# Kernel optimization log

Measured on AMD Instinct MI355X. Metric: run time of the kernel, lower is better.

The kernel has to match this reference:

```python
import jax, jax.numpy as jnp
import numpy as np

C = 512        # concept_num
D = 256        # input_dim / embedding_dim
H = 512        # msg_hidden_dim
M = 256        # msg_output_dim
OH = 512       # hidden_dim
T = 2          # edge_type_num
E = C * (C - 1)  # fully-connected graph without self-loops = 261632


def _glorot(key, shape, fan_in):
    return jax.random.normal(key, shape, jnp.float32) / np.sqrt(fan_in).astype(np.float32)


def setup_inputs() -> dict:
    key = jax.random.key(0)
    ks = jax.random.split(key, 12)
    inputs = jax.random.normal(ks[0], (C, D), jnp.float32)
    rel_type = jax.random.uniform(ks[1], (E, T), jnp.float32)
    send_idx = jax.random.randint(ks[2], (E,), 0, C, jnp.int32)
    rec_idx = jax.random.randint(ks[3], (E,), 0, C, jnp.int32)
    # per-edge-type message MLP params, stacked over type dim
    W1 = _glorot(ks[4], (T, 2 * D, H), 2 * D)
    b1 = jnp.zeros((T, H), jnp.float32)
    W2 = _glorot(ks[5], (T, H, M), H)
    b2 = jnp.zeros((T, M), jnp.float32)
    # output MLP params
    Wo1 = _glorot(ks[6], (M, OH), M)
    bo1 = jnp.zeros((OH,), jnp.float32)
    Wo2 = _glorot(ks[7], (OH, OH), OH)
    bo2 = jnp.zeros((OH,), jnp.float32)
    Wo3 = _glorot(ks[8], (OH, D), OH)
    bo3 = jnp.zeros((D,), jnp.float32)
    return {"inputs": inputs, "rel_type": rel_type, "W1": W1, "b1": b1,
            "W2": W2, "b2": b2, "Wo1": Wo1, "bo1": bo1, "Wo2": Wo2,
            "bo2": bo2, "Wo3": Wo3, "bo3": bo3,
            "send_idx": send_idx, "rec_idx": rec_idx}


def reference(inputs, rel_type, W1, b1, W2, b2, Wo1, bo1, Wo2, bo2, Wo3, bo3,
              send_idx, rec_idx):
    # node2edge: one-hot sparse matmul == index gather
    senders = jnp.take(inputs, send_idx, axis=0)      # [E, D]
    receivers = jnp.take(inputs, rec_idx, axis=0)     # [E, D]
    pre_msg = jnp.concatenate([senders, receivers], axis=-1)  # [E, 2D]
    # per-edge-type MLPs, weighted-summed by rel_type (dropout=0 / eval mode)
    all_msgs = jnp.zeros((pre_msg.shape[0], M), jnp.float32)
    for i in range(T):
        msg = jax.nn.relu(pre_msg @ W1[i] + b1[i])    # [E, H]
        msg = jax.nn.relu(msg @ W2[i] + b2[i])        # [E, M]
        all_msgs = all_msgs + msg * rel_type[:, i:i + 1]
    # edge2node: transposed one-hot sparse matmul == scatter-add over receivers
    agg_msgs = jax.ops.segment_sum(all_msgs, rec_idx, num_segments=inputs.shape[0])  # [C, M]
    pred = jax.nn.relu(agg_msgs @ Wo1 + bo1)
    pred = jax.nn.relu(pred @ Wo2 + bo2)
    return pred @ Wo3 + bo3                           # [C, D]
```

## Files before the change

kernel.cpp:

```cpp
#include <hip/hip_runtime.h>

#define C_N   512
#define E_N   261632
#define CAP   768

typedef _Float16 f16;
typedef _Float16 f16x8_t __attribute__((ext_vector_type(8)));
typedef float    f32x16_t __attribute__((ext_vector_type(16)));

__global__ __launch_bounds__(256) void k_prep_all(
    const float* __restrict__ inputs, const float* __restrict__ W1,
    const float* __restrict__ b1, const float* __restrict__ W2,
    const float* __restrict__ Wo1, const float* __restrict__ Wo2, const float* __restrict__ Wo3,
    f16* __restrict__ SA, f16* __restrict__ RB, f16* __restrict__ W2p,
    f16* __restrict__ Wo1p, f16* __restrict__ Wo2p, f16* __restrict__ Wo3p,
    int* __restrict__ cnt, float* __restrict__ agg)
{
  __shared__ f16 wt[2][256][18];
  int bid = blockIdx.x;
  int tid = threadIdx.x;
  if (bid < 64) {
    int lane = tid & 63, w = tid >> 6;
    int hlf = lane >> 5, l31 = lane & 31;
    int br = bid & 7, bc = (bid >> 3) & 1, mi = bid >> 4;
    int t = mi >> 1, half = mi & 1;
    const float* Wsrc = W1 + (size_t)t * 512 * 512 + (size_t)half * 256 * 512;

    f32x16_t acc[2][2];
    #pragma unroll
    for (int rt = 0; rt < 2; rt++)
      #pragma unroll
      for (int ctl = 0; ctl < 2; ctl++)
        #pragma unroll
        for (int r = 0; r < 16; r++) acc[rt][ctl][r] = 0.f;

    #pragma unroll
    for (int i = 0; i < 4; i++) {
      int idx = tid + i * 256;
      int k = idx >> 6, n4 = idx & 63;
      float4 v = *(const float4*)&Wsrc[(size_t)k * 512 + bc * 256 + n4 * 4];
      wt[0][n4 * 4 + 0][k] = (f16)v.x;
      wt[0][n4 * 4 + 1][k] = (f16)v.y;
      wt[0][n4 * 4 + 2][k] = (f16)v.z;
      wt[0][n4 * 4 + 3][k] = (f16)v.w;
    }

    for (int kc = 0; kc < 16; kc++) {
      __syncthreads();
      if (kc + 1 < 16) {
        int b = (kc + 1) & 1;
        #pragma unroll
        for (int i = 0; i < 4; i++) {
          int idx = tid + i * 256;
          int k = idx >> 6, n4 = idx & 63;
          float4 v = *(const float4*)&Wsrc[(size_t)((kc + 1) * 16 + k) * 512 + bc * 256 + n4 * 4];
          wt[b][n4 * 4 + 0][k] = (f16)v.x;
          wt[b][n4 * 4 + 1][k] = (f16)v.y;
          wt[b][n4 * 4 + 2][k] = (f16)v.z;
          wt[b][n4 * 4 + 3][k] = (f16)v.w;
        }
      }
      f16x8_t af[2];
      #pragma unroll
      for (int rt = 0; rt < 2; rt++) {
        const float4* p = (const float4*)&inputs[(size_t)(br * 64 + rt * 32 + l31) * 256 + kc * 16 + hlf * 8];
        float4 u0 = p[0], u1 = p[1];
        af[rt] = (f16x8_t){(f16)u0.x, (f16)u0.y, (f16)u0.z, (f16)u0.w,
                           (f16)u1.x, (f16)u1.y, (f16)u1.z, (f16)u1.w};
      }
      int b = kc & 1;
      #pragma unroll
      for (int ctl = 0; ctl < 2; ctl++) {
        int n = (2 * w + ctl) * 32 + l31;
        f16x8_t bfr = *(const f16x8_t*)&wt[b][n][hlf * 8];
        #pragma unroll
        for (int rt = 0; rt < 2; rt++)
          acc[rt][ctl] = __builtin_amdgcn_mfma_f32_32x32x16_f16(af[rt], bfr, acc[rt][ctl], 0, 0, 0);
      }
    }
    f16* dst = (half == 0) ? SA : RB;
    #pragma unroll
    for (int ctl = 0; ctl < 2; ctl++) {
      int col = bc * 256 + (2 * w + ctl) * 32 + l31;
      float bias = (half == 1) ? b1[t * 512 + col] : 0.f;
      #pragma unroll
      for (int rt = 0; rt < 2; rt++)
        #pragma unroll
        for (int r = 0; r < 16; r++) {
          int row = br * 64 + rt * 32 + (r & 3) + 8 * (r >> 2) + 4 * hlf;
          dst[((size_t)(t * 512 + row)) * 512 + col] = (f16)(acc[rt][ctl][r] + bias);
        }
    }
  } else if (bid < 192) {
    int gid  = (bid - 64) * 256 + tid;
    int lane = gid & 63;
    int ct   = (gid >> 6) & 7;
    int kc   = (gid >> 9) & 31;
    int t    = gid >> 14;
    int n    = ct * 32 + (lane & 31);
    int k0   = kc * 16 + (lane >> 5) * 8;
    const float* src = W2 + (size_t)t * 512 * 256;
    f16x8_t v;
    #pragma unroll
    for (int j = 0; j < 8; j++) v[j] = (f16)src[(size_t)(k0 + j) * 256 + n];
    *(f16x8_t*)(W2p + (size_t)gid * 8) = v;
  } else if (bid < 256) {
    int gid  = (bid - 192) * 256 + tid;
    int lane = gid & 63;
    int ct   = (gid >> 6) & 15;
    int kc   = gid >> 10;
    int n    = ct * 32 + (lane & 31);
    int k0   = kc * 16 + (lane >> 5) * 8;
    f16x8_t v;
    #pragma unroll
    for (int j = 0; j < 8; j++) v[j] = (f16)Wo1[(size_t)(k0 + j) * 512 + n];
    *(f16x8_t*)(Wo1p + (size_t)gid * 8) = v;
  } else if (bid < 384) {
    int gid  = (bid - 256) * 256 + tid;
    int lane = gid & 63;
    int ct   = (gid >> 6) & 15;
    int kc   = gid >> 10;
    int n    = ct * 32 + (lane & 31);
    int k0   = kc * 16 + (lane >> 5) * 8;
    f16x8_t v;
    #pragma unroll
    for (int j = 0; j < 8; j++) v[j] = (f16)Wo2[(size_t)(k0 + j) * 512 + n];
    *(f16x8_t*)(Wo2p + (size_t)gid * 8) = v;
  } else if (bid < 448) {
    int gid  = (bid - 384) * 256 + tid;
    int lane = gid & 63;
    int ct   = (gid >> 6) & 7;
    int kc   = gid >> 9;
    int n    = ct * 32 + (lane & 31);
    int k0   = kc * 16 + (lane >> 5) * 8;
    f16x8_t v;
    #pragma unroll
    for (int j = 0; j < 8; j++) v[j] = (f16)Wo3[(size_t)(k0 + j) * 256 + n];
    *(f16x8_t*)(Wo3p + (size_t)gid * 8) = v;
  } else if (bid == 448) {
    for (int i = tid; i < 512 * 16; i += 256) cnt[i] = 0;
  } else {
    float4* a4 = (float4*)agg;
    for (int i = tid; i < 512 * 64; i += 256) a4[i] = make_float4(0.f, 0.f, 0.f, 0.f);
  }
}

__global__ __launch_bounds__(512) void k_scatter_d(const int* __restrict__ rec,
    const int* __restrict__ send, const float* __restrict__ rel,
    int* __restrict__ cnt, uint2* __restrict__ smeta)
{
  __shared__ int lh[512];
  __shared__ int lb[512];
  int b = blockIdx.x;
  int e0 = b * (E_N / 128);
  lh[threadIdx.x] = 0;
  __syncthreads();
  for (int i = threadIdx.x; i < E_N / 128; i += 512)
    atomicAdd(&lh[rec[e0 + i]], 1);
  __syncthreads();
  {
    int c = lh[threadIdx.x];
    lb[threadIdx.x] = c ? atomicAdd(&cnt[threadIdx.x * 16], c) : 0;
    lh[threadIdx.x] = 0;
  }
  __syncthreads();
  for (int i = threadIdx.x; i < E_N / 128; i += 512) {
    int e = e0 + i;
    int r = rec[e];
    int p = r * CAP + lb[r] + atomicAdd(&lh[r], 1);
    f16 r0 = (f16)rel[2 * (size_t)e];
    f16 r1 = (f16)rel[2 * (size_t)e + 1];
    unsigned pk = ((unsigned)__builtin_bit_cast(unsigned short, r1) << 16)
                |  (unsigned)__builtin_bit_cast(unsigned short, r0);
    smeta[p] = make_uint2((unsigned)send[e], pk);
  }
}

#define H1S2 264

__global__ __launch_bounds__(512, 4) void k_edges(
    const f16* __restrict__ SA, const f16* __restrict__ RB,
    const f16* __restrict__ W2p, const float* __restrict__ b2,
    const uint2* __restrict__ smeta, const int* __restrict__ cnt,
    float* __restrict__ agg)
{
  __shared__ f16   h1[128 * H1S2];
  __shared__ f16   rbs[2][512];
  __shared__ float b2s[2][256];
  __shared__ float aggL[256];
  __shared__ float relv[128][2];
  __shared__ int   sends[128];

  int c   = blockIdx.x;
  int ti  = blockIdx.y;
  int n_c = cnt[c * 16];
  if (ti * 128 >= n_c) return;

  int tid  = threadIdx.x;
  int lane = tid & 63;
  int w    = tid >> 6;
  int hlf  = lane >> 5;
  int l31  = lane & 31;
  int q5   = tid & 31;
  int rb0  = tid >> 5;

  if (tid < 128) {
    int t = tid >> 6, qq = tid & 63;
    *(f16x8_t*)&rbs[t][qq * 8] = *(const f16x8_t*)&RB[((size_t)(t * 512 + c)) * 512 + qq * 8];
  }
  if (tid < 256) aggL[tid] = 0.0f;
  { int t = (tid >> 8) & 1, col = tid & 255; b2s[t][col] = b2[t * 256 + col]; }

  int s0 = c * CAP + ti * 128;
  int nv = n_c - ti * 128; if (nv > 128) nv = 128;

  if (tid < 128) {
    if (tid < nv) {
      uint2 m = smeta[s0 + tid];
      sends[tid] = (int)m.x;
      relv[tid][0] = (float)__builtin_bit_cast(f16, (unsigned short)(m.y & 0xffffu));
      relv[tid][1] = (float)__builtin_bit_cast(f16, (unsigned short)(m.y >> 16));
    } else {
      sends[tid] = 0; relv[tid][0] = 0.f; relv[tid][1] = 0.f;
    }
  }
  __syncthreads();

  f16x8_t g[8];
  const f16x8_t* SAc = (const f16x8_t*)SA;
  const f16x8_t* Bp  = (const f16x8_t*)W2p;
  f32x16_t acc[4];

  #pragma unroll
  for (int j = 0; j < 8; j++)
    g[j] = SAc[(size_t)sends[rb0 + 16 * j] * 64 + q5];

  for (int ph = 0; ph < 4; ph++) {
    int t  = ph >> 1;
    int kh = ph & 1;

    {
      f16x8_t rbq = *(const f16x8_t*)&rbs[t][(kh * 32 + q5) * 8];
      #pragma unroll
      for (int j = 0; j < 8; j++) {
        int row = rb0 + 16 * j;
        f16x8_t hv;
        #pragma unroll
        for (int e = 0; e < 8; e++) {
          f16 v = (f16)(g[j][e] + rbq[e]);
          hv[e] = (v > (f16)0.0f) ? v : (f16)0.0f;
        }
        *(f16x8_t*)&h1[row * H1S2 + q5 * 8] = hv;
      }
    }
    __syncthreads();

    if (kh == 0) {
      #pragma unroll
      for (int rt = 0; rt < 4; rt++)
        #pragma unroll
        for (int r = 0; r < 16; r++) acc[rt][r] = 0.f;
    }

    f16x8_t bb[2];
    bb[0] = Bp[(size_t)(((t * 32 + kh * 16 + 0) * 8 + w) * 64 + lane)];
    bb[1] = Bp[(size_t)(((t * 32 + kh * 16 + 1) * 8 + w) * 64 + lane)];

    if (ph < 3) {
      int tn  = (ph + 1) >> 1;
      int khn = (ph + 1) & 1;
      #pragma unroll
      for (int j = 0; j < 8; j++)
        g[j] = SAc[(size_t)(tn * 512 + sends[rb0 + 16 * j]) * 64 + khn * 32 + q5];
    }

    for (int kc = 0; kc < 16; kc++) {
      int pb = kc & 1;
      #pragma unroll
      for (int rt = 0; rt < 4; rt++) {
        f16x8_t af = *(const f16x8_t*)&h1[(rt * 32 + l31) * H1S2 + kc * 16 + hlf * 8];
        acc[rt] = __builtin_amdgcn_mfma_f32_32x32x16_f16(af, bb[pb], acc[rt], 0, 0, 0);
      }
      if (kc + 2 < 16)
        bb[pb] = Bp[(size_t)(((t * 32 + kh * 16 + kc + 2) * 8 + w) * 64 + lane)];
    }

    if (kh == 1) {
      int col = w * 32 + l31;
      float b2c = b2s[t][col];
      float csum = 0.0f;
      #pragma unroll
      for (int rt = 0; rt < 4; rt++)
        #pragma unroll
        for (int r = 0; r < 16; r++) {
          int row = rt * 32 + (r & 3) + 8 * (r >> 2) + 4 * hlf;
          float v = fmaxf(acc[rt][r] + b2c, 0.0f);
          csum += v * relv[row][t];
        }
      csum += __shfl_xor(csum, 32, 64);
      if (hlf == 0) aggL[col] += csum;
    }
    __syncthreads();
  }

  if (tid < 256) atomicAdd(&agg[(size_t)c * 256 + tid], aggL[tid]);
}

#define HOS 520

__global__ __launch_bounds__(512, 1) void k_omlp(const float* __restrict__ agg,
    const f16* __restrict__ Wo1p, const float* __restrict__ bo1,
    const f16* __restrict__ Wo2p, const float* __restrict__ bo2,
    const f16* __restrict__ Wo3p, const float* __restrict__ bo3,
    float* __restrict__ out)
{
  __shared__ f16 hL1[32 * HOS];
  __shared__ f16 hL2[32 * HOS];
  int tid = threadIdx.x, lane = tid & 63, w = tid >> 6;
  int hlf = lane >> 5, l31 = lane & 31;
  int br = blockIdx.x;

  {
    f32x16_t acc[2];
    #pragma unroll
    for (int ctl = 0; ctl < 2; ctl++)
      #pragma unroll
      for (int r = 0; r < 16; r++) acc[ctl][r] = 0.f;
    for (int kc = 0; kc < 16; kc++) {
      const float4* p = (const float4*)&agg[(size_t)(br * 32 + l31) * 256 + kc * 16 + hlf * 8];
      float4 u0 = p[0], u1 = p[1];
      f16x8_t af = (f16x8_t){(f16)u0.x, (f16)u0.y, (f16)u0.z, (f16)u0.w,
                             (f16)u1.x, (f16)u1.y, (f16)u1.z, (f16)u1.w};
      #pragma unroll
      for (int ctl = 0; ctl < 2; ctl++) {
        int ct = 2 * w + ctl;
        f16x8_t bfr = *(const f16x8_t*)&Wo1p[((size_t)(kc * 16 + ct) * 64 + lane) * 8];
        acc[ctl] = __builtin_amdgcn_mfma_f32_32x32x16_f16(af, bfr, acc[ctl], 0, 0, 0);
      }
    }
    #pragma unroll
    for (int ctl = 0; ctl < 2; ctl++) {
      int col = (2 * w + ctl) * 32 + l31;
      float bias = bo1[col];
      #pragma unroll
      for (int r = 0; r < 16; r++) {
        int row = (r & 3) + 8 * (r >> 2) + 4 * hlf;
        hL1[row * HOS + col] = (f16)fmaxf(acc[ctl][r] + bias, 0.f);
      }
    }
  }
  __syncthreads();

  {
    f32x16_t acc[2];
    #pragma unroll
    for (int ctl = 0; ctl < 2; ctl++)
      #pragma unroll
      for (int r = 0; r < 16; r++) acc[ctl][r] = 0.f;
    for (int kc = 0; kc < 32; kc++) {
      f16x8_t af = *(const f16x8_t*)&hL1[l31 * HOS + kc * 16 + hlf * 8];
      #pragma unroll
      for (int ctl = 0; ctl < 2; ctl++) {
        int ct = 2 * w + ctl;
        f16x8_t bfr = *(const f16x8_t*)&Wo2p[((size_t)(kc * 16 + ct) * 64 + lane) * 8];
        acc[ctl] = __builtin_amdgcn_mfma_f32_32x32x16_f16(af, bfr, acc[ctl], 0, 0, 0);
      }
    }
    #pragma unroll
    for (int ctl = 0; ctl < 2; ctl++) {
      int col = (2 * w + ctl) * 32 + l31;
      float bias = bo2[col];
      #pragma unroll
      for (int r = 0; r < 16; r++) {
        int row = (r & 3) + 8 * (r >> 2) + 4 * hlf;
        hL2[row * HOS + col] = (f16)fmaxf(acc[ctl][r] + bias, 0.f);
      }
    }
  }
  __syncthreads();

  {
    f32x16_t acc;
    #pragma unroll
    for (int r = 0; r < 16; r++) acc[r] = 0.f;
    for (int kc = 0; kc < 32; kc++) {
      f16x8_t af  = *(const f16x8_t*)&hL2[l31 * HOS + kc * 16 + hlf * 8];
      f16x8_t bfr = *(const f16x8_t*)&Wo3p[((size_t)(kc * 8 + w) * 64 + lane) * 8];
      acc = __builtin_amdgcn_mfma_f32_32x32x16_f16(af, bfr, acc, 0, 0, 0);
    }
    int col = w * 32 + l31;
    float bias = bo3[col];
    #pragma unroll
    for (int r = 0; r < 16; r++) {
      int row = br * 32 + (r & 3) + 8 * (r >> 2) + 4 * hlf;
      out[(size_t)row * 256 + col] = acc[r] + bias;
    }
  }
}

extern "C" void kernel_launch(void* const* d_in, const int* in_sizes, int n_in,
                              void* d_out, int out_size, void* d_ws, size_t ws_size,
                              hipStream_t stream)
{
  (void)in_sizes; (void)n_in; (void)out_size; (void)ws_size;
  const float* inputs = (const float*)d_in[0];
  const float* rel    = (const float*)d_in[1];
  const float* W1     = (const float*)d_in[2];
  const float* b1     = (const float*)d_in[3];
  const float* W2     = (const float*)d_in[4];
  const float* b2     = (const float*)d_in[5];
  const float* Wo1    = (const float*)d_in[6];
  const float* bo1    = (const float*)d_in[7];
  const float* Wo2    = (const float*)d_in[8];
  const float* bo2    = (const float*)d_in[9];
  const float* Wo3    = (const float*)d_in[10];
  const float* bo3    = (const float*)d_in[11];
  const int* send_idx = (const int*)d_in[12];
  const int* rec_idx  = (const int*)d_in[13];
  float* out = (float*)d_out;

  char* ws = (char*)d_ws;
  f16*    SA    = (f16*)   (ws);
  f16*    RB    = (f16*)   (ws + (1024u << 10));
  f16*    W2p   = (f16*)   (ws + (2048u << 10));
  float*  agg   = (float*) (ws + (2560u << 10));
  int*    cnt   = (int*)   (ws + (3072u << 10));
  f16*    Wo1p  = (f16*)   (ws + (3136u << 10));
  f16*    Wo2p  = (f16*)   (ws + (3392u << 10));
  f16*    Wo3p  = (f16*)   (ws + (3904u << 10));
  uint2*  smeta = (uint2*) (ws + (4160u << 10));

  k_prep_all <<<dim3(450),    dim3(256), 0, stream>>>(inputs, W1, b1, W2, Wo1, Wo2, Wo3,
                                                      SA, RB, W2p, Wo1p, Wo2p, Wo3p, cnt, agg);
  k_scatter_d<<<dim3(128),    dim3(512), 0, stream>>>(rec_idx, send_idx, rel, cnt, smeta);
  k_edges    <<<dim3(512, 5), dim3(512), 0, stream>>>(SA, RB, W2p, b2, smeta, cnt, agg);
  k_omlp     <<<dim3(16),     dim3(512), 0, stream>>>(agg, Wo1p, bo1, Wo2p, bo2, Wo3p, bo3, out);
}
```

Before: 298.9 us.

## Fold edge bucketing into prep kernel and use 2x2 MFMA wave tiling

The edge-bucketing scatter kernel is merged into the prep kernel as 128 extra 256-thread blocks, and the count buffer is cleared with hipMemsetAsync beforehand. This removes one kernel launch and lets the bucketing run alongside the weight conversion. In k_edges, each wave now computes a 64-row by 64-column tile instead of 128 by 32. Each A fragment read from LDS then feeds two MFMAs, which cuts LDS traffic. The cost is twice the B-fragment global loads per wave, more accumulator registers, and a second per-row-group aggL buffer.

```diff
diff --git a/kernel.cpp b/kernel.cpp
--- a/kernel.cpp
+++ b/kernel.cpp
@@ -12,9 +12,10 @@
     const float* __restrict__ inputs, const float* __restrict__ W1,
     const float* __restrict__ b1, const float* __restrict__ W2,
     const float* __restrict__ Wo1, const float* __restrict__ Wo2, const float* __restrict__ Wo3,
+    const int* __restrict__ rec, const int* __restrict__ send, const float* __restrict__ rel,
     f16* __restrict__ SA, f16* __restrict__ RB, f16* __restrict__ W2p,
     f16* __restrict__ Wo1p, f16* __restrict__ Wo2p, f16* __restrict__ Wo3p,
-    int* __restrict__ cnt, float* __restrict__ agg)
+    int* __restrict__ cnt, float* __restrict__ agg, uint2* __restrict__ smeta)
 {
   __shared__ f16 wt[2][256][18];
   int bid = blockIdx.x;
@@ -138,41 +139,34 @@
     for (int j = 0; j < 8; j++) v[j] = (f16)Wo3[(size_t)(k0 + j) * 256 + n];
     *(f16x8_t*)(Wo3p + (size_t)gid * 8) = v;
   } else if (bid == 448) {
-    for (int i = tid; i < 512 * 16; i += 256) cnt[i] = 0;
-  } else {
     float4* a4 = (float4*)agg;
     for (int i = tid; i < 512 * 64; i += 256) a4[i] = make_float4(0.f, 0.f, 0.f, 0.f);
-  }
-}
-
-__global__ __launch_bounds__(512) void k_scatter_d(const int* __restrict__ rec,
-    const int* __restrict__ send, const float* __restrict__ rel,
-    int* __restrict__ cnt, uint2* __restrict__ smeta)
-{
-  __shared__ int lh[512];
-  __shared__ int lb[512];
-  int b = blockIdx.x;
-  int e0 = b * (E_N / 128);
-  lh[threadIdx.x] = 0;
-  __syncthreads();
-  for (int i = threadIdx.x; i < E_N / 128; i += 512)
-    atomicAdd(&lh[rec[e0 + i]], 1);
-  __syncthreads();
-  {
-    int c = lh[threadIdx.x];
-    lb[threadIdx.x] = c ? atomicAdd(&cnt[threadIdx.x * 16], c) : 0;
-    lh[threadIdx.x] = 0;
-  }
-  __syncthreads();
-  for (int i = threadIdx.x; i < E_N / 128; i += 512) {
-    int e = e0 + i;
-    int r = rec[e];
-    int p = r * CAP + lb[r] + atomicAdd(&lh[r], 1);
-    f16 r0 = (f16)rel[2 * (size_t)e];
-    f16 r1 = (f16)rel[2 * (size_t)e + 1];
-    unsigned pk = ((unsigned)__builtin_bit_cast(unsigned short, r1) << 16)
-                |  (unsigned)__builtin_bit_cast(unsigned short, r0);
-    smeta[p] = make_uint2((unsigned)send[e], pk);
+  } else {
+    __shared__ int lh[512];
+    __shared__ int lb[512];
+    int b = bid - 449;
+    int e0 = b * (E_N / 128);
+    for (int i = tid; i < 512; i += 256) lh[i] = 0;
+    __syncthreads();
+    for (int i = tid; i < E_N / 128; i += 256)
+      atomicAdd(&lh[rec[e0 + i]], 1);
+    __syncthreads();
+    for (int i = tid; i < 512; i += 256) {
+      int c = lh[i];
+      lb[i] = c ? atomicAdd(&cnt[i * 16], c) : 0;
+      lh[i] = 0;
+    }
+    __syncthreads();
+    for (int i = tid; i < E_N / 128; i += 256) {
+      int e = e0 + i;
+      int r = rec[e];
+      int p = r * CAP + lb[r] + atomicAdd(&lh[r], 1);
+      f16 r0 = (f16)rel[2 * (size_t)e];
+      f16 r1 = (f16)rel[2 * (size_t)e + 1];
+      unsigned pk = ((unsigned)__builtin_bit_cast(unsigned short, r1) << 16)
+                  |  (unsigned)__builtin_bit_cast(unsigned short, r0);
+      smeta[p] = make_uint2((unsigned)send[e], pk);
+    }
   }
 }
 
@@ -187,7 +181,7 @@
   __shared__ f16   h1[128 * H1S2];
   __shared__ f16   rbs[2][512];
   __shared__ float b2s[2][256];
-  __shared__ float aggL[256];
+  __shared__ float aggL[2][256];
   __shared__ float relv[128][2];
   __shared__ int   sends[128];
 
@@ -199,6 +193,8 @@
   int tid  = threadIdx.x;
   int lane = tid & 63;
   int w    = tid >> 6;
+  int rg   = w & 1;
+  int wc   = w >> 1;
   int hlf  = lane >> 5;
   int l31  = lane & 31;
   int q5   = tid & 31;
@@ -208,7 +204,7 @@
     int t = tid >> 6, qq = tid & 63;
     *(f16x8_t*)&rbs[t][qq * 8] = *(const f16x8_t*)&RB[((size_t)(t * 512 + c)) * 512 + qq * 8];
   }
-  if (tid < 256) aggL[tid] = 0.0f;
+  aggL[tid >> 8][tid & 255] = 0.0f;
   { int t = (tid >> 8) & 1, col = tid & 255; b2s[t][col] = b2[t * 256 + col]; }
 
   int s0 = c * CAP + ti * 128;
@@ -229,7 +225,7 @@
   f16x8_t g[8];
   const f16x8_t* SAc = (const f16x8_t*)SA;
   const f16x8_t* Bp  = (const f16x8_t*)W2p;
-  f32x16_t acc[4];
+  f32x16_t acc[2][2];
 
   #pragma unroll
   for (int j = 0; j < 8; j++)
@@ -257,14 +253,19 @@
 
     if (kh == 0) {
       #pragma unroll
-      for (int rt = 0; rt < 4; rt++)
-        #pragma unroll
-        for (int r = 0; r < 16; r++) acc[rt][r] = 0.f;
-    }
-
-    f16x8_t bb[2];
-    bb[0] = Bp[(size_t)(((t * 32 + kh * 16 + 0) * 8 + w) * 64 + lane)];
-    bb[1] = Bp[(size_t)(((t * 32 + kh * 16 + 1) * 8 + w) * 64 + lane)];
+      for (int rt = 0; rt < 2; rt++)
+        #pragma unroll
+        for (int ctl = 0; ctl < 2; ctl++)
+          #pragma unroll
+          for (int r = 0; r < 16; r++) acc[rt][ctl][r] = 0.f;
+    }
+
+    f16x8_t bb[2][2];
+    #pragma unroll
+    for (int ctl = 0; ctl < 2; ctl++) {
+      bb[0][ctl] = Bp[(size_t)(((t * 32 + kh * 16 + 0) * 8 + 2 * wc + ctl) * 64 + lane)];
+      bb[1][ctl] = Bp[(size_t)(((t * 32 + kh * 16 + 1) * 8 + 2 * wc + ctl) * 64 + lane)];
+    }
 
     if (ph < 3) {
       int tn  = (ph + 1) >> 1;
@@ -277,33 +278,41 @@
     for (int kc = 0; kc < 16; kc++) {
       int pb = kc & 1;
       #pragma unroll
-      for (int rt = 0; rt < 4; rt++) {
-        f16x8_t af = *(const f16x8_t*)&h1[(rt * 32 + l31) * H1S2 + kc * 16 + hlf * 8];
-        acc[rt] = __builtin_amdgcn_mfma_f32_32x32x16_f16(af, bb[pb], acc[rt], 0, 0, 0);
-      }
-      if (kc + 2 < 16)
-        bb[pb] = Bp[(size_t)(((t * 32 + kh * 16 + kc + 2) * 8 + w) * 64 + lane)];
+      for (int rt = 0; rt < 2; rt++) {
+        f16x8_t af = *(const f16x8_t*)&h1[(rg * 64 + rt * 32 + l31) * H1S2 + kc * 16 + hlf * 8];
+        #pragma unroll
+        for (int ctl = 0; ctl < 2; ctl++)
+          acc[rt][ctl] = __builtin_amdgcn_mfma_f32_32x32x16_f16(af, bb[pb][ctl], acc[rt][ctl], 0, 0, 0);
+      }
+      if (kc + 2 < 16) {
+        #pragma unroll
+        for (int ctl = 0; ctl < 2; ctl++)
+          bb[pb][ctl] = Bp[(size_t)(((t * 32 + kh * 16 + kc + 2) * 8 + 2 * wc + ctl) * 64 + lane)];
+      }
     }
 
     if (kh == 1) {
-      int col = w * 32 + l31;
-      float b2c = b2s[t][col];
-      float csum = 0.0f;
-      #pragma unroll
-      for (int rt = 0; rt < 4; rt++)
-        #pragma unroll
-        for (int r = 0; r < 16; r++) {
-          int row = rt * 32 + (r & 3) + 8 * (r >> 2) + 4 * hlf;
-          float v = fmaxf(acc[rt][r] + b2c, 0.0f);
-          csum += v * relv[row][t];
-        }
-      csum += __shfl_xor(csum, 32, 64);
-      if (hlf == 0) aggL[col] += csum;
+      #pragma unroll
+      for (int ctl = 0; ctl < 2; ctl++) {
+        int col = (2 * wc + ctl) * 32 + l31;
+        float b2c = b2s[t][col];
+        float csum = 0.0f;
+        #pragma unroll
+        for (int rt = 0; rt < 2; rt++)
+          #pragma unroll
+          for (int r = 0; r < 16; r++) {
+            int row = rg * 64 + rt * 32 + (r & 3) + 8 * (r >> 2) + 4 * hlf;
+            float v = fmaxf(acc[rt][ctl][r] + b2c, 0.0f);
+            csum += v * relv[row][t];
+          }
+        csum += __shfl_xor(csum, 32, 64);
+        if (hlf == 0) aggL[rg][col] += csum;
+      }
     }
     __syncthreads();
   }
 
-  if (tid < 256) atomicAdd(&agg[(size_t)c * 256 + tid], aggL[tid]);
+  if (tid < 256) atomicAdd(&agg[(size_t)c * 256 + tid], aggL[0][tid] + aggL[1][tid]);
 }
 
 #define HOS 520
@@ -430,9 +439,11 @@
   f16*    Wo3p  = (f16*)   (ws + (3904u << 10));
   uint2*  smeta = (uint2*) (ws + (4160u << 10));
 
-  k_prep_all <<<dim3(450),    dim3(256), 0, stream>>>(inputs, W1, b1, W2, Wo1, Wo2, Wo3,
-                                                      SA, RB, W2p, Wo1p, Wo2p, Wo3p, cnt, agg);
-  k_scatter_d<<<dim3(128),    dim3(512), 0, stream>>>(rec_idx, send_idx, rel, cnt, smeta);
+  hipMemsetAsync(cnt, 0, 512 * 16 * sizeof(int), stream);
+  k_prep_all <<<dim3(577),    dim3(256), 0, stream>>>(inputs, W1, b1, W2, Wo1, Wo2, Wo3,
+                                                      rec_idx, send_idx, rel,
+                                                      SA, RB, W2p, Wo1p, Wo2p, Wo3p,
+                                                      cnt, agg, smeta);
   k_edges    <<<dim3(512, 5), dim3(512), 0, stream>>>(SA, RB, W2p, b2, smeta, cnt, agg);
   k_omlp     <<<dim3(16),     dim3(512), 0, stream>>>(agg, Wo1p, bo1, Wo2p, bo2, Wo3p, bo3, out);
 }
```

New measurement: 319.4 us. +6.9%, slower.
